# Kernel tuning notes

Measured on AMD Instinct MI355X. Metric: run time of the kernel, lower is better.

Reference implementation:

```python
import jax, jax.numpy as jnp
import numpy as np

H = 128  # GRU hidden size


def gru_cell(x_t, h, W_ih, W_hh, b_ih, b_hh):
    # Standard torch GRU cell math.
    gi = x_t @ W_ih.T + b_ih            # (bs, 3H)
    gh = h @ W_hh.T + b_hh              # (bs, 3H)
    i_r, i_z, i_n = jnp.split(gi, 3, axis=-1)
    h_r, h_z, h_n = jnp.split(gh, 3, axis=-1)
    r = jax.nn.sigmoid(i_r + h_r)
    z = jax.nn.sigmoid(i_z + h_z)
    n = jnp.tanh(i_n + r * h_n)
    return (1.0 - z) * n + z * h


def setup_inputs() -> dict:
    key = jax.random.key(0)
    ks = jax.random.split(key, 16)
    bs, seq, emb, nc = 64, 1024, 300, 23
    s = 0.05
    inp = {
        "x": jax.random.normal(ks[0], (bs, seq, emb), jnp.float32),
        "adj": jax.random.uniform(ks[1], (bs, seq, seq), jnp.float32),
        "mask": jax.random.uniform(ks[2], (bs, seq, 1), jnp.float32),
        # GRU forward direction params (torch layout: W_ih (3H, emb), W_hh (3H, H))
        "W_ih_f": jax.random.normal(ks[3], (3 * H, emb), jnp.float32) * s,
        "W_hh_f": jax.random.normal(ks[4], (3 * H, H), jnp.float32) * s,
        "b_ih_f": jax.random.normal(ks[5], (3 * H,), jnp.float32) * s,
        "b_hh_f": jax.random.normal(ks[6], (3 * H,), jnp.float32) * s,
        # GRU backward direction params
        "W_ih_b": jax.random.normal(ks[7], (3 * H, emb), jnp.float32) * s,
        "W_hh_b": jax.random.normal(ks[8], (3 * H, H), jnp.float32) * s,
        "b_ih_b": jax.random.normal(ks[9], (3 * H,), jnp.float32) * s,
        "b_hh_b": jax.random.normal(ks[10], (3 * H,), jnp.float32) * s,
        # MLP head: Linear(300+256,128) -> Linear(128,64) -> Linear(64,23)
        "W1": jax.random.normal(ks[11], (128, emb + 2 * H), jnp.float32) * s,
        "b1": jnp.zeros((128,), jnp.float32),
        "W2": jax.random.normal(ks[12], (64, 128), jnp.float32) * s,
        "b2": jnp.zeros((64,), jnp.float32),
        "W3": jax.random.normal(ks[13], (nc, 64), jnp.float32) * s,
        "b3": jnp.zeros((nc,), jnp.float32),
    }
    return inp


def reference(x, adj, mask, W_ih_f, W_hh_f, b_ih_f, b_hh_f,
              W_ih_b, W_hh_b, b_ih_b, b_hh_b, W1, b1, W2, b2, W3, b3):
    x = x * mask                                   # (bs, seq, emb)
    bs, seq, emb = x.shape

    # --- bidirectional GRU, last-step output ---
    # Forward direction output at t = seq-1 is the final hidden of a full scan.
    h0 = jnp.zeros((bs, H), x.dtype)
    def step(h, x_t):
        h_new = gru_cell(x_t, h, W_ih_f, W_hh_f, b_ih_f, b_hh_f)
        return h_new, None
    h_fwd, _ = jax.lax.scan(step, h0, jnp.swapaxes(x, 0, 1))  # (bs, H)
    # Backward direction output at t = seq-1 is exactly ONE cell step on x[:, -1]
    # starting from the zero initial state (it has only consumed the last token).
    h_bwd = gru_cell(x[:, -1, :], h0, W_ih_b, W_hh_b, b_ih_b, b_hh_b)
    h = jnp.concatenate([h_fwd, h_bwd], axis=1)    # (bs, 2H)

    # --- gfm: sum_{i,j} x_i * x_j per feature == (sum_i x_i)^2 ---
    # (original code materializes a (bs, seq*seq, emb) tensor; adj is dead code)
    s = jnp.sum(x, axis=1)                         # (bs, emb)
    gfm = s * s                                    # (bs, emb)

    # --- MLP head (dropout is identity at eval) ---
    z = jnp.concatenate([h, gfm], axis=1)          # (bs, 2H + emb)
    z = jax.nn.relu(z @ W1.T + b1)
    z = jax.nn.relu(z @ W2.T + b2)
    logit = z @ W3.T + b3                          # (bs, num_class)
    return logit
```

## Files before the change

kernel.cpp:

```cpp
#include <hip/hip_runtime.h>
#include <hip/hip_bf16.h>

#define HH   128
#define EMB  300
#define SEQ  1024
#define BS   64
#define NG   384
#define NCHUNK 8

typedef __attribute__((ext_vector_type(8))) short  bf16x8;
typedef __attribute__((ext_vector_type(4))) float  f32x4;
typedef _Float16 f16x2 __attribute__((ext_vector_type(2)));

__device__ __forceinline__ unsigned short f2bf(float f) {
    unsigned int u = __float_as_uint(f);
    unsigned int r = (u + 0x7fffu + ((u >> 16) & 1u)) >> 16;
    return (unsigned short)r;
}
__device__ __forceinline__ float fexp(float x) { return __builtin_amdgcn_exp2f(x * 1.44269504088896f); }
__device__ __forceinline__ float fsig(float x) { return __builtin_amdgcn_rcpf(1.f + fexp(-x)); }
__device__ __forceinline__ float ftanh(float x){ return __builtin_amdgcn_rcpf(1.f + fexp(-2.f*x)) * 2.f - 1.f; }

#define BAR_LDS() asm volatile("s_waitcnt lgkmcnt(0)\n\ts_barrier" ::: "memory")

__global__ __launch_bounds__(256) void gi_gemm(const float* __restrict__ X,
                                               const float* __restrict__ mask,
                                               const float* __restrict__ W,
                                               const float* __restrict__ bias,
                                               float* __restrict__ out) {
    __shared__ __align__(16) unsigned short As[128 * 32];
    __shared__ __align__(16) unsigned short Bs[128 * 32];
    const int m0   = blockIdx.x * 128;
    const int n0   = blockIdx.y * 128;
    const int tid  = threadIdx.x;
    const int row  = tid >> 1;
    const int seg  = tid & 1;
    const int wave = tid >> 6;
    const int lane = tid & 63;
    const int wr   = wave >> 1, wc = wave & 1;
    const int r16  = lane & 15, kg = lane >> 4;

    f32x4 acc[4][4];
    #pragma unroll
    for (int m = 0; m < 4; ++m)
        #pragma unroll
        for (int n = 0; n < 4; ++n) acc[m][n] = (f32x4){0.f,0.f,0.f,0.f};

    const float mrow = mask[m0 + row];

    for (int k0 = 0; k0 < 320; k0 += 32) {
        {
            const float* src = X + (size_t)(m0 + row) * EMB + k0 + seg * 16;
            unsigned short tmp[16];
            if (k0 + seg * 16 + 15 < EMB) {
                #pragma unroll
                for (int i = 0; i < 4; ++i) {
                    float4 v = ((const float4*)src)[i];
                    tmp[i*4+0] = f2bf(v.x * mrow);
                    tmp[i*4+1] = f2bf(v.y * mrow);
                    tmp[i*4+2] = f2bf(v.z * mrow);
                    tmp[i*4+3] = f2bf(v.w * mrow);
                }
            } else {
                #pragma unroll
                for (int i = 0; i < 16; ++i) {
                    int c = k0 + seg * 16 + i;
                    float v = (c < EMB) ? src[i] : 0.f;
                    tmp[i] = f2bf(v * mrow);
                }
            }
            uint4* dst = (uint4*)&As[row * 32 + seg * 16];
            dst[0] = ((const uint4*)tmp)[0];
            dst[1] = ((const uint4*)tmp)[1];
        }
        {
            const float* src = W + (size_t)(n0 + row) * EMB + k0 + seg * 16;
            unsigned short tmp[16];
            if (k0 + seg * 16 + 15 < EMB) {
                #pragma unroll
                for (int i = 0; i < 4; ++i) {
                    float4 v = ((const float4*)src)[i];
                    tmp[i*4+0] = f2bf(v.x);
                    tmp[i*4+1] = f2bf(v.y);
                    tmp[i*4+2] = f2bf(v.z);
                    tmp[i*4+3] = f2bf(v.w);
                }
            } else {
                #pragma unroll
                for (int i = 0; i < 16; ++i) {
                    int c = k0 + seg * 16 + i;
                    float v = (c < EMB) ? src[i] : 0.f;
                    tmp[i] = f2bf(v);
                }
            }
            uint4* dst = (uint4*)&Bs[row * 32 + seg * 16];
            dst[0] = ((const uint4*)tmp)[0];
            dst[1] = ((const uint4*)tmp)[1];
        }
        __syncthreads();

        bf16x8 a[4], bfr[4];
        #pragma unroll
        for (int m = 0; m < 4; ++m)
            a[m] = *(const bf16x8*)&As[(wr * 64 + m * 16 + r16) * 32 + kg * 8];
        #pragma unroll
        for (int n = 0; n < 4; ++n)
            bfr[n] = *(const bf16x8*)&Bs[(wc * 64 + n * 16 + r16) * 32 + kg * 8];
        #pragma unroll
        for (int m = 0; m < 4; ++m)
            #pragma unroll
            for (int n = 0; n < 4; ++n)
                acc[m][n] = __builtin_amdgcn_mfma_f32_16x16x32_bf16(a[m], bfr[n], acc[m][n], 0, 0, 0);
        __syncthreads();
    }

    #pragma unroll
    for (int m = 0; m < 4; ++m) {
        const int rowb = m0 + wr * 64 + m * 16 + (lane >> 4) * 4;
        #pragma unroll
        for (int n = 0; n < 4; ++n) {
            const int col = n0 + wc * 64 + n * 16 + r16;
            const float bj = bias[col];
            #pragma unroll
            for (int q = 0; q < 4; ++q)
                out[(size_t)(rowb + q) * NG + col] = acc[m][n][q] + bj;
        }
    }
}

__global__ __launch_bounds__(320) void col_sum(const float* __restrict__ X,
                                               const float* __restrict__ mask,
                                               float* __restrict__ spart) {
    const int b = blockIdx.x, c = blockIdx.y;
    const int e = threadIdx.x;
    if (e >= EMB) return;
    const int tchunk = SEQ / NCHUNK;
    float acc = 0.f;
    const float* xb = X + ((size_t)b * SEQ + (size_t)c * tchunk) * EMB;
    const float* mb = mask + (size_t)b * SEQ + (size_t)c * tchunk;
    for (int t = 0; t < tchunk; ++t)
        acc += xb[(size_t)t * EMB + e] * mb[t];
    spart[((size_t)b * NCHUNK + c) * EMB + e] = acc;
}

__global__ __launch_bounds__(256, 1) void gru_scan(const float* __restrict__ gi,
                                                   const float* __restrict__ Whh,
                                                   const float* __restrict__ bhh,
                                                   float* __restrict__ hout) {
    const int b    = blockIdx.x;
    const int tid  = threadIdx.x;
    const int j    = tid >> 1;
    const int half = tid & 1;
    __shared__ __align__(16) _Float16 hb[2][HH];

    f16x2 wr_[32], wz_[32], wn_[32];
    {
        const float2* r0 = (const float2*)(Whh + (size_t)j * HH            + half * 64);
        const float2* r1 = (const float2*)(Whh + (size_t)(j + HH) * HH     + half * 64);
        const float2* r2 = (const float2*)(Whh + (size_t)(j + 2 * HH) * HH + half * 64);
        #pragma unroll
        for (int i = 0; i < 32; ++i) {
            float2 a = r0[i], c = r1[i], d = r2[i];
            wr_[i] = (f16x2){(_Float16)a.x, (_Float16)a.y};
            wz_[i] = (f16x2){(_Float16)c.x, (_Float16)c.y};
            wn_[i] = (f16x2){(_Float16)d.x, (_Float16)d.y};
        }
    }
    const float br_ = bhh[j], bz_ = bhh[j + HH], bn_ = bhh[j + 2 * HH];

    float hreg = 0.f;
    if (tid < HH) hb[0][tid] = (_Float16)0.f;
    const float* gb = gi + (size_t)b * SEQ * NG;

    float gAr, gAz, gAn, gBr, gBz, gBn, gCr, gCz, gCn, gDr, gDz, gDn;
    {
        const float* g0 = gb;               gAr = g0[j]; gAz = g0[j+HH]; gAn = g0[j+2*HH];
        const float* g1 = gb + NG;          gBr = g1[j]; gBz = g1[j+HH]; gBn = g1[j+2*HH];
        const float* g2 = gb + 2 * NG;      gCr = g2[j]; gCz = g2[j+HH]; gCn = g2[j+2*HH];
        const float* g3 = gb + 3 * NG;      gDr = g3[j]; gDz = g3[j+HH]; gDn = g3[j+2*HH];
    }
    BAR_LDS();

#define GRU_BODY(P, GR, GZ, GN, TOFF)                                          \
    {                                                                          \
        float ar = 0.f, az = 0.f, an = 0.f;                                    \
        const uint4* hp = (const uint4*)&hb[P][half * 64];                     \
        _Pragma("unroll")                                                      \
        for (int i = 0; i < 8; ++i) {                                          \
            union { uint4 u; f16x2 h2[4]; } U;                                 \
            U.u = hp[i];                                                       \
            _Pragma("unroll")                                                  \
            for (int k = 0; k < 4; ++k) {                                      \
                ar = __builtin_amdgcn_fdot2(wr_[i*4+k], U.h2[k], ar, false);   \
                az = __builtin_amdgcn_fdot2(wz_[i*4+k], U.h2[k], az, false);   \
                an = __builtin_amdgcn_fdot2(wn_[i*4+k], U.h2[k], an, false);   \
            }                                                                  \
        }                                                                      \
        ar += __shfl_xor(ar, 1);                                               \
        az += __shfl_xor(az, 1);                                               \
        an += __shfl_xor(an, 1);                                               \
        const float r = fsig(GR + ar + br_);                                   \
        const float z = fsig(GZ + az + bz_);                                   \
        const float n = ftanh(GN + r * (an + bn_));                            \
        hreg = (1.f - z) * n + z * hreg;                                       \
        hb[P ^ 1][j] = (_Float16)hreg;                                         \
        const float* gnext = gb + (size_t)(t + (TOFF) + 4) * NG;               \
        GR = gnext[j]; GZ = gnext[j + HH]; GN = gnext[j + 2 * HH];              \
        BAR_LDS();                                                             \
    }

    for (int t = 0; t < SEQ; t += 4) {
        GRU_BODY(0, gAr, gAz, gAn, 0)
        GRU_BODY(1, gBr, gBz, gBn, 1)
        GRU_BODY(0, gCr, gCz, gCn, 2)
        GRU_BODY(1, gDr, gDz, gDn, 3)
    }
#undef GRU_BODY
    if (!half) hout[b * HH + j] = hreg;
}

__global__ __launch_bounds__(384) void gru_bwd(const float* __restrict__ X,
                                               const float* __restrict__ mask,
                                               const float* __restrict__ Wih,
                                               const float* __restrict__ bih,
                                               const float* __restrict__ bhh,
                                               float* __restrict__ hout) {
    const int b = blockIdx.x, j = threadIdx.x;
    __shared__ float gib[NG];
    const float* xr = X + ((size_t)b * SEQ + (SEQ - 1)) * EMB;
    const float  mv = mask[(size_t)b * SEQ + SEQ - 1];
    const float* wr_ = Wih + (size_t)j * EMB;
    float acc = 0.f;
    for (int e = 0; e < EMB; ++e) acc += xr[e] * wr_[e];
    gib[j] = acc * mv + bih[j];
    __syncthreads();
    if (j < HH) {
        const float r = fsig(gib[j] + bhh[j]);
        const float z = fsig(gib[j + HH] + bhh[j + HH]);
        const float n = ftanh(gib[j + 2 * HH] + r * bhh[j + 2 * HH]);
        hout[b * HH + j] = (1.f - z) * n;
    }
}

__global__ __launch_bounds__(128) void mlp(const float* __restrict__ hf,
                                           const float* __restrict__ hb,
                                           const float* __restrict__ spart,
                                           const float* __restrict__ W1, const float* __restrict__ b1,
                                           const float* __restrict__ W2, const float* __restrict__ b2,
                                           const float* __restrict__ W3, const float* __restrict__ b3,
                                           float* __restrict__ out) {
    const int b = blockIdx.x, j = threadIdx.x;
    __shared__ float zin[2 * HH + EMB];
    __shared__ float l1[128];
    __shared__ float l2[64];
    zin[j]      = hf[b * HH + j];
    zin[HH + j] = hb[b * HH + j];
    for (int e = j; e < EMB; e += 128) {
        float v = 0.f;
        #pragma unroll
        for (int c = 0; c < NCHUNK; ++c)
            v += spart[((size_t)b * NCHUNK + c) * EMB + e];
        zin[2 * HH + e] = v * v;
    }
    __syncthreads();
    {
        float a = b1[j];
        const float* w = W1 + (size_t)j * (2 * HH + EMB);
        for (int i = 0; i < 2 * HH + EMB; ++i) a += zin[i] * w[i];
        l1[j] = fmaxf(a, 0.f);
    }
    __syncthreads();
    if (j < 64) {
        float a = b2[j];
        const float* w = W2 + (size_t)j * 128;
        for (int i = 0; i < 128; ++i) a += l1[i] * w[i];
        l2[j] = fmaxf(a, 0.f);
    }
    __syncthreads();
    if (j < 23) {
        float a = b3[j];
        const float* w = W3 + (size_t)j * 64;
        for (int i = 0; i < 64; ++i) a += l2[i] * w[i];
        out[b * 23 + j] = a;
    }
}

extern "C" void kernel_launch(void* const* d_in, const int* in_sizes, int n_in,
                              void* d_out, int out_size, void* d_ws, size_t ws_size,
                              hipStream_t stream) {
    const float* x     = (const float*)d_in[0];
    const float* mask  = (const float*)d_in[2];
    const float* Wih_f = (const float*)d_in[3];
    const float* Whh_f = (const float*)d_in[4];
    const float* bih_f = (const float*)d_in[5];
    const float* bhh_f = (const float*)d_in[6];
    const float* Wih_b = (const float*)d_in[7];
    const float* bih_b = (const float*)d_in[9];
    const float* bhh_b = (const float*)d_in[10];
    const float* W1 = (const float*)d_in[11];
    const float* b1 = (const float*)d_in[12];
    const float* W2 = (const float*)d_in[13];
    const float* b2 = (const float*)d_in[14];
    const float* W3 = (const float*)d_in[15];
    const float* b3 = (const float*)d_in[16];
    float* out = (float*)d_out;

    float* gi    = (float*)d_ws;
    float* spart = gi + (size_t)BS * SEQ * NG;
    float* hf    = spart + (size_t)BS * NCHUNK * EMB;
    float* hb    = hf + BS * HH;

    gi_gemm<<<dim3(512, 3), dim3(256), 0, stream>>>(x, mask, Wih_f, bih_f, gi);
    col_sum<<<dim3(BS, NCHUNK), dim3(320), 0, stream>>>(x, mask, spart);
    gru_scan<<<dim3(BS), dim3(256), 0, stream>>>(gi, Whh_f, bhh_f, hf);
    gru_bwd<<<dim3(BS), dim3(384), 0, stream>>>(x, mask, Wih_b, bih_b, bhh_b, hb);
    mlp<<<dim3(BS), dim3(128), 0, stream>>>(hf, hb, spart, W1, b1, W2, b2, W3, b3, out);
}
```

Before: 585.0 us.

## Batch 16 sequences per block in GRU scan using MFMA for recurrent matmul

The recurrent scan now processes 16 batch rows per 512-thread block (4 blocks total) and computes the h·W_hh product with 16x16x32 f16 MFMA instead of per-thread fdot2 loops over one sequence per block. The r/z hidden biases are folded into the input-gate GEMM epilogue to cut per-step adds. This raises per-step compute efficiency but uses only 4 CUs instead of 64, so per-step latency (barrier, MFMA chain, gate math for 4 outputs per lane) decides whether the serial loop gets shorter.

```diff
diff --git a/kernel.cpp b/kernel.cpp
--- a/kernel.cpp
+++ b/kernel.cpp
@@ -11,6 +11,7 @@
 typedef __attribute__((ext_vector_type(8))) short  bf16x8;
 typedef __attribute__((ext_vector_type(4))) float  f32x4;
 typedef _Float16 f16x2 __attribute__((ext_vector_type(2)));
+typedef _Float16 f16x8 __attribute__((ext_vector_type(8)));
 
 __device__ __forceinline__ unsigned short f2bf(float f) {
     unsigned int u = __float_as_uint(f);
@@ -27,6 +28,7 @@
                                                const float* __restrict__ mask,
                                                const float* __restrict__ W,
                                                const float* __restrict__ bias,
+                                               const float* __restrict__ bhh2,
                                                float* __restrict__ out) {
     __shared__ __align__(16) unsigned short As[128 * 32];
     __shared__ __align__(16) unsigned short Bs[128 * 32];
@@ -120,7 +122,7 @@
         #pragma unroll
         for (int n = 0; n < 4; ++n) {
             const int col = n0 + wc * 64 + n * 16 + r16;
-            const float bj = bias[col];
+            const float bj = bias[col] + (col < 2 * HH ? bhh2[col] : 0.f);
             #pragma unroll
             for (int q = 0; q < 4; ++q)
                 out[(size_t)(rowb + q) * NG + col] = acc[m][n][q] + bj;
@@ -143,80 +145,93 @@
     spart[((size_t)b * NCHUNK + c) * EMB + e] = acc;
 }
 
-__global__ __launch_bounds__(256, 1) void gru_scan(const float* __restrict__ gi,
+__global__ __launch_bounds__(512, 1) void gru_scan(const float* __restrict__ gi,
                                                    const float* __restrict__ Whh,
                                                    const float* __restrict__ bhh,
                                                    float* __restrict__ hout) {
-    const int b    = blockIdx.x;
     const int tid  = threadIdx.x;
-    const int j    = tid >> 1;
-    const int half = tid & 1;
-    __shared__ __align__(16) _Float16 hb[2][HH];
-
-    f16x2 wr_[32], wz_[32], wn_[32];
+    const int w    = tid >> 6;
+    const int lane = tid & 63;
+    const int m16  = lane & 15;
+    const int kg   = lane >> 4;
+    const int bg   = blockIdx.x * 16 + m16;
+    const int j0   = w * 16 + kg * 4;
+
+    __shared__ _Float16 hl[2][16][136];
+
+    f16x8 wfr[4], wfz[4], wfn[4];
     {
-        const float2* r0 = (const float2*)(Whh + (size_t)j * HH            + half * 64);
-        const float2* r1 = (const float2*)(Whh + (size_t)(j + HH) * HH     + half * 64);
-        const float2* r2 = (const float2*)(Whh + (size_t)(j + 2 * HH) * HH + half * 64);
-        #pragma unroll
-        for (int i = 0; i < 32; ++i) {
-            float2 a = r0[i], c = r1[i], d = r2[i];
-            wr_[i] = (f16x2){(_Float16)a.x, (_Float16)a.y};
-            wz_[i] = (f16x2){(_Float16)c.x, (_Float16)c.y};
-            wn_[i] = (f16x2){(_Float16)d.x, (_Float16)d.y};
+        const float* base = Whh + (size_t)(w * 16 + m16) * HH + kg * 8;
+        #pragma unroll
+        for (int ks = 0; ks < 4; ++ks) {
+            float4 a0 = *(const float4*)(base + ks * 32);
+            float4 a1 = *(const float4*)(base + ks * 32 + 4);
+            wfr[ks] = (f16x8){(_Float16)a0.x,(_Float16)a0.y,(_Float16)a0.z,(_Float16)a0.w,
+                              (_Float16)a1.x,(_Float16)a1.y,(_Float16)a1.z,(_Float16)a1.w};
+            a0 = *(const float4*)(base + HH * HH + ks * 32);
+            a1 = *(const float4*)(base + HH * HH + ks * 32 + 4);
+            wfz[ks] = (f16x8){(_Float16)a0.x,(_Float16)a0.y,(_Float16)a0.z,(_Float16)a0.w,
+                              (_Float16)a1.x,(_Float16)a1.y,(_Float16)a1.z,(_Float16)a1.w};
+            a0 = *(const float4*)(base + 2 * HH * HH + ks * 32);
+            a1 = *(const float4*)(base + 2 * HH * HH + ks * 32 + 4);
+            wfn[ks] = (f16x8){(_Float16)a0.x,(_Float16)a0.y,(_Float16)a0.z,(_Float16)a0.w,
+                              (_Float16)a1.x,(_Float16)a1.y,(_Float16)a1.z,(_Float16)a1.w};
         }
     }
-    const float br_ = bhh[j], bz_ = bhh[j + HH], bn_ = bhh[j + 2 * HH];
-
-    float hreg = 0.f;
-    if (tid < HH) hb[0][tid] = (_Float16)0.f;
-    const float* gb = gi + (size_t)b * SEQ * NG;
-
-    float gAr, gAz, gAn, gBr, gBz, gBn, gCr, gCz, gCn, gDr, gDz, gDn;
-    {
-        const float* g0 = gb;               gAr = g0[j]; gAz = g0[j+HH]; gAn = g0[j+2*HH];
-        const float* g1 = gb + NG;          gBr = g1[j]; gBz = g1[j+HH]; gBn = g1[j+2*HH];
-        const float* g2 = gb + 2 * NG;      gCr = g2[j]; gCz = g2[j+HH]; gCn = g2[j+2*HH];
-        const float* g3 = gb + 3 * NG;      gDr = g3[j]; gDz = g3[j+HH]; gDn = g3[j+2*HH];
-    }
+    float bn[4];
+    #pragma unroll
+    for (int q = 0; q < 4; ++q) bn[q] = bhh[2 * HH + j0 + q];
+
+    for (int i = tid; i < 16 * 136; i += 512) ((unsigned short*)hl[0])[i] = 0;
+    float hq[4] = {0.f, 0.f, 0.f, 0.f};
+
+    const float* p0 = gi + ((size_t)bg * SEQ + 0) * NG + j0;
+    const float* p1 = gi + ((size_t)bg * SEQ + 1) * NG + j0;
+    f32x4 Gr0 = *(const f32x4*)(p0);
+    f32x4 Gz0 = *(const f32x4*)(p0 + HH);
+    f32x4 Gn0 = *(const f32x4*)(p0 + 2 * HH);
+    f32x4 Gr1 = *(const f32x4*)(p1);
+    f32x4 Gz1 = *(const f32x4*)(p1 + HH);
+    f32x4 Gn1 = *(const f32x4*)(p1 + 2 * HH);
+    p0 += 2 * NG; p1 += 2 * NG;
     BAR_LDS();
 
-#define GRU_BODY(P, GR, GZ, GN, TOFF)                                          \
+#define GRU_BODY(P, GR, GZ, GN, PP)                                            \
     {                                                                          \
-        float ar = 0.f, az = 0.f, an = 0.f;                                    \
-        const uint4* hp = (const uint4*)&hb[P][half * 64];                     \
+        f32x4 aR = (f32x4){0.f,0.f,0.f,0.f};                                   \
+        f32x4 aZ = (f32x4){0.f,0.f,0.f,0.f};                                   \
+        f32x4 aN = (f32x4){0.f,0.f,0.f,0.f};                                   \
         _Pragma("unroll")                                                      \
-        for (int i = 0; i < 8; ++i) {                                          \
-            union { uint4 u; f16x2 h2[4]; } U;                                 \
-            U.u = hp[i];                                                       \
-            _Pragma("unroll")                                                  \
-            for (int k = 0; k < 4; ++k) {                                      \
-                ar = __builtin_amdgcn_fdot2(wr_[i*4+k], U.h2[k], ar, false);   \
-                az = __builtin_amdgcn_fdot2(wz_[i*4+k], U.h2[k], az, false);   \
-                an = __builtin_amdgcn_fdot2(wn_[i*4+k], U.h2[k], an, false);   \
-            }                                                                  \
+        for (int ks = 0; ks < 4; ++ks) {                                       \
+            f16x8 hbf = *(const f16x8*)&hl[P][m16][ks * 32 + kg * 8];          \
+            aR = __builtin_amdgcn_mfma_f32_16x16x32_f16(wfr[ks], hbf, aR, 0, 0, 0); \
+            aZ = __builtin_amdgcn_mfma_f32_16x16x32_f16(wfz[ks], hbf, aZ, 0, 0, 0); \
+            aN = __builtin_amdgcn_mfma_f32_16x16x32_f16(wfn[ks], hbf, aN, 0, 0, 0); \
         }                                                                      \
-        ar += __shfl_xor(ar, 1);                                               \
-        az += __shfl_xor(az, 1);                                               \
-        an += __shfl_xor(an, 1);                                               \
-        const float r = fsig(GR + ar + br_);                                   \
-        const float z = fsig(GZ + az + bz_);                                   \
-        const float n = ftanh(GN + r * (an + bn_));                            \
-        hreg = (1.f - z) * n + z * hreg;                                       \
-        hb[P ^ 1][j] = (_Float16)hreg;                                         \
-        const float* gnext = gb + (size_t)(t + (TOFF) + 4) * NG;               \
-        GR = gnext[j]; GZ = gnext[j + HH]; GN = gnext[j + 2 * HH];              \
+        union { _Float16 h[4]; uint2 u; } HU;                                  \
+        _Pragma("unroll")                                                      \
+        for (int q = 0; q < 4; ++q) {                                          \
+            const float r  = fsig(GR[q] + aR[q]);                              \
+            const float zz = fsig(GZ[q] + aZ[q]);                              \
+            const float nn = ftanh(GN[q] + r * (aN[q] + bn[q]));               \
+            hq[q] = nn + zz * (hq[q] - nn);                                    \
+            HU.h[q] = (_Float16)hq[q];                                         \
+        }                                                                      \
+        *(uint2*)&hl[P ^ 1][m16][j0] = HU.u;                                   \
+        GR = *(const f32x4*)(PP);                                              \
+        GZ = *(const f32x4*)(PP + HH);                                         \
+        GN = *(const f32x4*)(PP + 2 * HH);                                     \
+        PP += 2 * NG;                                                          \
         BAR_LDS();                                                             \
     }
 
-    for (int t = 0; t < SEQ; t += 4) {
-        GRU_BODY(0, gAr, gAz, gAn, 0)
-        GRU_BODY(1, gBr, gBz, gBn, 1)
-        GRU_BODY(0, gCr, gCz, gCn, 2)
-        GRU_BODY(1, gDr, gDz, gDn, 3)
+    for (int it = 0; it < SEQ / 2; ++it) {
+        GRU_BODY(0, Gr0, Gz0, Gn0, p0)
+        GRU_BODY(1, Gr1, Gz1, Gn1, p1)
     }
 #undef GRU_BODY
-    if (!half) hout[b * HH + j] = hreg;
+
+    *(float4*)&hout[(size_t)bg * HH + j0] = (float4){hq[0], hq[1], hq[2], hq[3]};
 }
 
 __global__ __launch_bounds__(384) void gru_bwd(const float* __restrict__ X,
@@ -310,9 +325,9 @@
     float* hf    = spart + (size_t)BS * NCHUNK * EMB;
     float* hb    = hf + BS * HH;
 
-    gi_gemm<<<dim3(512, 3), dim3(256), 0, stream>>>(x, mask, Wih_f, bih_f, gi);
+    gi_gemm<<<dim3(512, 3), dim3(256), 0, stream>>>(x, mask, Wih_f, bih_f, bhh_f, gi);
     col_sum<<<dim3(BS, NCHUNK), dim3(320), 0, stream>>>(x, mask, spart);
-    gru_scan<<<dim3(BS), dim3(256), 0, stream>>>(gi, Whh_f, bhh_f, hf);
+    gru_scan<<<dim3(4), dim3(512), 0, stream>>>(gi, Whh_f, bhh_f, hf);
     gru_bwd<<<dim3(BS), dim3(384), 0, stream>>>(x, mask, Wih_b, bih_b, bhh_b, hb);
     mlp<<<dim3(BS), dim3(128), 0, stream>>>(hf, hb, spart, W1, b1, W2, b2, W3, b3, out);
 }
```

Result: slower. 812.2 us (+38.8%).
